# Performance work log

Hardware: AMD Instinct MI355X
Metric: run time of the kernel (lower is better)

## Reference

```python
import jax, jax.numpy as jnp
import numpy as np

# Clebsch-Gordan coefficients in the real basis; l=1 components stored in (y,z,x) order
S2 = 1.0 / np.sqrt(2.0)
S3 = 1.0 / np.sqrt(3.0)
S6 = 1.0 / np.sqrt(6.0)
_C2 = np.zeros((5, 3, 3), np.float32)
_C2[0, 2, 0] = _C2[0, 0, 2] = S2          # ~ xy
_C2[1, 0, 1] = _C2[1, 1, 0] = S2          # ~ yz
_C2[2, 1, 1] = 2.0 * S6                   # ~ 2z^2 - x^2 - y^2
_C2[2, 2, 2] = -S6
_C2[2, 0, 0] = -S6
_C2[3, 2, 1] = _C2[3, 1, 2] = S2          # ~ xz
_C2[4, 2, 2] = S2                          # ~ x^2 - y^2
_C2[4, 0, 0] = -S2
C2 = jnp.asarray(_C2)

N0, N1 = 64, 32        # multiplicities of input 0e / 1o irreps
CUTOFF = 5.0


def basis_functions(pos):
    """pos [N,3] -> (scalars [N,64], l=1 features [N,32,3])."""
    r = jnp.linalg.norm(pos, axis=-1, keepdims=True) + 1e-9        # [N,1]
    d = pos[:, (1, 2, 0)] / r                                       # unit dir, (y,z,x) order
    c0 = jnp.linspace(0.0, CUTOFF, N0, dtype=pos.dtype)
    c1 = jnp.linspace(0.0, CUTOFF, N1, dtype=pos.dtype)
    f0 = jnp.exp(-4.0 * (r - c0) ** 2)                              # [N,64] gaussian RBF
    f1 = jnp.exp(-4.0 * (r - c1) ** 2)                              # [N,32]
    x1 = f1[:, :, None] * d[:, None, :]                             # [N,32,3]
    return f0, x1


def lin_l(x, W):
    # channel mixing within one irrep block; preserves the m axis if present
    if x.ndim == 2:
        return x @ W
    return jnp.einsum('ncm,cd->ndm', x, W)


def tensor_product(a0, a1, b0, b1):
    """Full uvw CG tensor product of (64x0 + 32x1) x (64x0 + 32x1)."""
    N = a0.shape[0]
    # l=0 outputs: 0x0->0 and 1x1->0
    p000 = jnp.einsum('na,nb->nab', a0, b0).reshape(N, -1)                 # [N,4096]
    p110 = jnp.einsum('nam,nbm->nab', a1, b1).reshape(N, -1) * S3          # [N,1024]
    t0 = jnp.concatenate([p000, p110], axis=1)                             # [N,5120]
    # l=1 outputs: 0x1->1, 1x0->1, 1x1->1 (cross product)
    p011 = (a0[:, :, None, None] * b1[:, None, :, :]).reshape(N, -1, 3)    # [N,2048,3]
    p101 = (a1[:, :, None, :] * b0[:, None, :, None]).reshape(N, -1, 3)    # [N,2048,3]
    p111 = (jnp.cross(a1[:, :, None, :], b1[:, None, :, :]) * S2).reshape(N, -1, 3)
    t1 = jnp.concatenate([p011, p101, p111], axis=1)                       # [N,5120,3]
    # l=2 output: 1x1->2 via CG tensor
    t2 = jnp.einsum('nai,nbj,mij->nabm', a1, b1, C2).reshape(N, -1, 5)     # [N,1024,5]
    return t0, t1, t2


def setup_inputs() -> dict:
    key = jax.random.key(0)
    ks = jax.random.split(key, 10)
    N = 4096
    def w(k, i, o):
        return jax.random.normal(k, (i, o), jnp.float32) / np.sqrt(i)
    return {
        'positions': jax.random.normal(ks[0], (N, 3), jnp.float32) * 2.0,
        'W1_0': w(ks[1], 64, 64),
        'W1_1': w(ks[2], 32, 32),
        'W2_0': w(ks[3], 64, 64),
        'W2_1': w(ks[4], 32, 32),
        'W3_0': w(ks[5], 5120, 64),
        'W3_1': w(ks[6], 5120, 32),
        'W3_2': w(ks[7], 1024, 16),
        'W_out': w(ks[8], 240, 7),
        'b_out': jnp.zeros((7,), jnp.float32),
    }


def reference(positions, W1_0, W1_1, W2_0, W2_1, W3_0, W3_1, W3_2, W_out, b_out):
    f0, f1 = basis_functions(positions)                 # 64x0, 32x1
    a0, a1 = lin_l(f0, W1_0), lin_l(f1, W1_1)           # linear1
    b0, b1 = lin_l(f0, W2_0), lin_l(f1, W2_1)           # linear2
    t0, t1, t2 = tensor_product(a0, a1, b0, b1)         # 5120x0, 5120x1, 1024x2
    y0 = lin_l(t0, W3_0)                                # [N,64]
    y1 = lin_l(t1, W3_1)                                # [N,32,3]
    y2 = lin_l(t2, W3_2)                                # [N,16,5]
    N = y0.shape[0]
    feat = jnp.concatenate([y0, y1.reshape(N, -1), y2.reshape(N, -1)], axis=1)  # [N,240]
    return feat @ W_out + b_out                         # [N,7]
```

## Files before the change

### kernel.cpp

```cpp
#include <hip/hip_runtime.h>
#include <math.h>

#define NS2 0.70710678118654752440f
#define NS3 0.57735026918962576451f
#define NS6 0.40824829046386301636f

typedef _Float16 f16;
typedef _Float16 f16x8 __attribute__((ext_vector_type(8)));
typedef float    f32x4 __attribute__((ext_vector_type(4)));

#define GT_K    22528
#define UV_ROW  216
#define OFF_UV  360448
#define OFF_IDX 1245184

__global__ __launch_bounds__(256) void prep_kernel(
    const float* __restrict__ pos,
    const float* __restrict__ W1_0, const float* __restrict__ W1_1,
    const float* __restrict__ W2_0, const float* __restrict__ W2_1,
    const float* __restrict__ W3_0, const float* __restrict__ W3_1,
    const float* __restrict__ W3_2, const float* __restrict__ Wout,
    const float* __restrict__ bout,
    f16* __restrict__ wsh, float* __restrict__ out, int N)
{
    __shared__ float smem[2464];
    const int tid = threadIdx.x;

    if (blockIdx.x < 88) {
        float* s_wo = smem;
        for (int i = tid; i < 1680; i += 256) s_wo[i] = Wout[i];
        __syncthreads();
        int k = blockIdx.x * 256 + tid;
        float acc[7] = {0.f,0.f,0.f,0.f,0.f,0.f,0.f};
        if (k < 4096) {
            int a = k >> 6, b = k & 63;
            const float* wr = W3_0 + (a*64 + b) * 64;
            #pragma unroll 4
            for (int o = 0; o < 64; o += 4) {
                float4 wv = *(const float4*)(wr + o);
                const float* w0 = s_wo + o * 7;
                #pragma unroll
                for (int kk = 0; kk < 7; ++kk)
                    acc[kk] = fmaf(wv.x, w0[kk], fmaf(wv.y, w0[7+kk],
                              fmaf(wv.z, w0[14+kk], fmaf(wv.w, w0[21+kk], acc[kk]))));
            }
        } else if (k < 10240) {
            int it = k >> 6, s = it - 64, m = s >> 5, a2 = s & 31, l = k & 63;
            const float* wr = W3_1 + (2048 + a2*64 + l) * 32;
            #pragma unroll 4
            for (int o = 0; o < 32; o += 4) {
                float4 wv = *(const float4*)(wr + o);
                const float* w0 = s_wo + (64 + o*3 + m) * 7;
                #pragma unroll
                for (int kk = 0; kk < 7; ++kk)
                    acc[kk] = fmaf(wv.x, w0[kk], fmaf(wv.y, w0[21+kk],
                              fmaf(wv.z, w0[42+kk], fmaf(wv.w, w0[63+kk], acc[kk]))));
            }
        } else {
            int it2 = (k - 10240) >> 5, l32 = k & 31;
            if (it2 < 32) {
                const float* wr = W3_0 + (4096 + it2*32 + l32) * 64;
                #pragma unroll 4
                for (int o = 0; o < 64; o += 4) {
                    float4 wv = *(const float4*)(wr + o);
                    const float* w0 = s_wo + o * 7;
                    #pragma unroll
                    for (int kk = 0; kk < 7; ++kk)
                        acc[kk] = fmaf(wv.x, w0[kk], fmaf(wv.y, w0[7+kk],
                                  fmaf(wv.z, w0[14+kk], fmaf(wv.w, w0[21+kk], acc[kk]))));
                }
            } else if (it2 < 224) {
                int t = it2 - 32, m = t >> 6, a = t & 63;
                const float* wr = W3_1 + (a*32 + l32) * 32;
                #pragma unroll 4
                for (int o = 0; o < 32; o += 4) {
                    float4 wv = *(const float4*)(wr + o);
                    const float* w0 = s_wo + (64 + o*3 + m) * 7;
                    #pragma unroll
                    for (int kk = 0; kk < 7; ++kk)
                        acc[kk] = fmaf(wv.x, w0[kk], fmaf(wv.y, w0[21+kk],
                                  fmaf(wv.z, w0[42+kk], fmaf(wv.w, w0[63+kk], acc[kk]))));
                }
            } else {
                int t = it2 - 224, m = t >> 5, a = t & 31;
                const float* wr = W3_2 + (a*32 + l32) * 16;
                #pragma unroll 4
                for (int o = 0; o < 16; o += 4) {
                    float4 wv = *(const float4*)(wr + o);
                    const float* w0 = s_wo + (160 + o*5 + m) * 7;
                    #pragma unroll
                    for (int kk = 0; kk < 7; ++kk)
                        acc[kk] = fmaf(wv.x, w0[kk], fmaf(wv.y, w0[35+kk],
                                  fmaf(wv.z, w0[70+kk], fmaf(wv.w, w0[105+kk], acc[kk]))));
                }
            }
        }
        #pragma unroll
        for (int r = 0; r < 7; ++r)  wsh[(size_t)r * GT_K + k] = (f16)acc[r];
        #pragma unroll
        for (int r = 7; r < 16; ++r) wsh[(size_t)r * GT_K + k] = (f16)0.f;
        return;
    }

    if (blockIdx.x == 88 + 512) {
        for (int c = tid; c < 704; c += 256) {
            int uidx, gidx;
            if (c < 320) {
                int it = c >> 1;
                if (it < 64) { uidx = it; gidx = 9; }
                else { int s = it - 64; uidx = 64 + (s & 31); gidx = s >> 5; }
            } else {
                int it2 = c - 320;
                if (it2 < 32)       { uidx = 64 + it2;                gidx = 3; }
                else if (it2 < 224) { int t = it2 - 32;  uidx = t & 63;       gidx = t >> 6; }
                else                { int t = it2 - 224; uidx = 64 + (t & 31); gidx = 4 + (t >> 5); }
            }
            ((unsigned short*)(wsh + OFF_IDX))[c] = (unsigned short)(uidx | (gidx << 8));
        }
        return;
    }

    float* s_f0 = smem;
    float* s_f1 = smem + 512;
    const int g8   = blockIdx.x - 88;
    const int base = g8 * 8;
    f16* uv = wsh + OFF_UV;
    {
        int d = tid & 63;
        #pragma unroll
        for (int jj = 0; jj < 2; ++jj) {
            int j = (tid >> 6) + jj * 4;
            int n = base + j;
            float px = pos[n*3+0], py = pos[n*3+1], pz = pos[n*3+2];
            float r  = sqrtf(px*px + py*py + pz*pz) + 1e-9f;
            float t0 = r - (5.0f/63.0f) * (float)d;
            s_f0[j*64 + d] = __expf(-4.f * t0 * t0);
        }
        {
            int j = tid >> 5, d1 = tid & 31;
            int n = base + j;
            float px = pos[n*3+0], py = pos[n*3+1], pz = pos[n*3+2];
            float r  = sqrtf(px*px + py*py + pz*pz) + 1e-9f;
            float t1 = r - (5.0f/31.0f) * (float)d1;
            s_f1[j*32 + d1] = __expf(-4.f * t1 * t1);
        }
        if (tid < 8) {
            int n = base + tid;
            float px = pos[n*3+0], py = pos[n*3+1], pz = pos[n*3+2];
            float r  = sqrtf(px*px + py*py + pz*pz) + 1e-9f;
            float iv = 1.0f / r;
            float d0 = py*iv, d1 = pz*iv, d2 = px*iv;
            f16* row = uv + (size_t)n * UV_ROW;
            row[192+0] = (f16)d0;
            row[192+1] = (f16)d1;
            row[192+2] = (f16)d2;
            row[192+3] = (f16)(NS3 * (d0*d0 + d1*d1 + d2*d2));
            row[192+4] = (f16)(2.f*NS2*d2*d0);
            row[192+5] = (f16)(2.f*NS2*d0*d1);
            row[192+6] = (f16)(NS6*(2.f*d1*d1 - d2*d2 - d0*d0));
            row[192+7] = (f16)(2.f*NS2*d2*d1);
            row[192+8] = (f16)(NS2*(d2*d2 - d0*d0));
            row[201]   = (f16)1.0f;
        }
        if (tid < 56) out[base*7 + tid] = bout[tid % 7];
    }
    __syncthreads();
    {
        int c = tid & 63, jb = tid >> 6;
        float aa0 = 0.f, aa1 = 0.f, ba0 = 0.f, ba1 = 0.f;
        const float* wa = W1_0 + c;
        const float* wb = W2_0 + c;
        #pragma unroll 4
        for (int d = 0; d < 64; ++d) {
            float wav = wa[d*64], wbv = wb[d*64];
            float fA = s_f0[jb*64 + d], fB = s_f0[(jb+4)*64 + d];
            aa0 = fmaf(fA, wav, aa0);  aa1 = fmaf(fB, wav, aa1);
            ba0 = fmaf(fA, wbv, ba0);  ba1 = fmaf(fB, wbv, ba1);
        }
        uv[(size_t)(base+jb  )*UV_ROW +      c] = (f16)aa0;
        uv[(size_t)(base+jb+4)*UV_ROW +      c] = (f16)aa1;
        uv[(size_t)(base+jb  )*UV_ROW + 96 + c] = (f16)ba0;
        uv[(size_t)(base+jb+4)*UV_ROW + 96 + c] = (f16)ba1;

        int c1 = tid & 31, j8 = tid >> 5;
        float aA = 0.f, aB = 0.f;
        const float* wA = W1_1 + c1;
        const float* wB = W2_1 + c1;
        #pragma unroll 4
        for (int d = 0; d < 32; ++d) {
            float f = s_f1[j8*32 + d];
            aA = fmaf(f, wA[d*32], aA);
            aB = fmaf(f, wB[d*32], aB);
        }
        uv[(size_t)(base+j8)*UV_ROW +  64 + c1] = (f16)aA;
        uv[(size_t)(base+j8)*UV_ROW + 160 + c1] = (f16)aB;
    }
}

__global__ __launch_bounds__(256) void main_kernel(
    const f16* __restrict__ wsh, float* __restrict__ out, int N)
{
    __shared__ f16 s_g[2][16][264];
    __shared__ f16 s_uv[64][UV_ROW];
    __shared__ f16 s_ugt[2][64][8];
    __shared__ unsigned short s_idx[704];

    const int tid  = threadIdx.x;
    const int w    = tid >> 6;
    const int lane = tid & 63;
    const int lq   = lane >> 4;
    const int lm   = lane & 15;
    const int g    = blockIdx.x >> 3;
    const int kq   = blockIdx.x & 7;

    {
        const uint4* src = (const uint4*)(wsh + OFF_UV + (size_t)g * 64 * UV_ROW);
        uint4* dst = (uint4*)&s_uv[0][0];
        for (int j = tid; j < 1728; j += 256) dst[j] = src[j];
        const unsigned int* isrc = (const unsigned int*)(wsh + OFF_IDX);
        unsigned int* idst = (unsigned int*)s_idx;
        for (int j = tid; j < 352; j += 256) idst[j] = isrc[j];
    }
    __syncthreads();

    const f16* myrow = &s_uv[w*16 + lm][0];
    f16x8 vA0 = *(const f16x8*)(myrow +  96 + lq*8);
    f16x8 vA1 = *(const f16x8*)(myrow + 128 + lq*8);
    f16x8 vB  = *(const f16x8*)(myrow + 160 + lq*8);

    auto c0_of = [&](int t) {
        return (t < 5) ? (kq*40 + t*8) : (320 + kq*48 + (t-5)*8);
    };
    auto stage = [&](int t, int buf) {
        int c0 = c0_of(t), k0 = c0 * 32;
        const f16* src = wsh + k0;
        for (int j = tid; j < 512; j += 256) {
            int row = j >> 5, col = j & 31;
            uint4 v = *(const uint4*)(src + (size_t)row * GT_K + col*8);
            *(uint4*)&s_g[buf][row][col*8] = v;
        }
        for (int j = tid; j < 512; j += 256) {
            int n = j >> 3, s = j & 7;
            unsigned short ix = s_idx[c0 + s];
            float u  = (float)s_uv[n][ix & 255];
            float gg = (float)s_uv[n][192 + (ix >> 8)];
            s_ugt[buf][n][s] = (f16)(u * gg);
        }
    };

    f32x4 acc = {0.f, 0.f, 0.f, 0.f};
    auto compute = [&](int buf, bool isA) {
        #pragma unroll
        for (int s = 0; s < 8; ++s) {
            f16x8 a = *(const f16x8*)&s_g[buf][lm][s*32 + lq*8];
            f16 ug  = s_ugt[buf][w*16 + lm][s];
            f16x8 vv = isA ? ((s & 1) ? vA1 : vA0) : vB;
            f16x8 b;
            #pragma unroll
            for (int j2 = 0; j2 < 8; ++j2) b[j2] = vv[j2] * ug;
            acc = __builtin_amdgcn_mfma_f32_16x16x32_f16(a, b, acc, 0, 0, 0);
        }
    };

    stage(0, 0);
    __syncthreads();
    for (int t = 0; t < 11; ++t) {
        int buf = t & 1;
        if (t < 10) stage(t + 1, buf ^ 1);
        compute(buf, t < 5);
        __syncthreads();
    }

    int node = g*64 + w*16 + lm;
    if (lq == 0) {
        #pragma unroll
        for (int r = 0; r < 4; ++r) atomicAdd(&out[node*7 + r], acc[r]);
    } else if (lq == 1) {
        #pragma unroll
        for (int r = 0; r < 3; ++r) atomicAdd(&out[node*7 + 4 + r], acc[r]);
    }
}

extern "C" void kernel_launch(void* const* d_in, const int* in_sizes, int n_in,
                              void* d_out, int out_size, void* d_ws, size_t ws_size,
                              hipStream_t stream)
{
    const float* pos  = (const float*)d_in[0];
    const float* W1_0 = (const float*)d_in[1];
    const float* W1_1 = (const float*)d_in[2];
    const float* W2_0 = (const float*)d_in[3];
    const float* W2_1 = (const float*)d_in[4];
    const float* W3_0 = (const float*)d_in[5];
    const float* W3_1 = (const float*)d_in[6];
    const float* W3_2 = (const float*)d_in[7];
    const float* Wout = (const float*)d_in[8];
    const float* bout = (const float*)d_in[9];
    f16*   wsh = (f16*)d_ws;
    float* op  = (float*)d_out;
    int N = in_sizes[0] / 3;

    prep_kernel<<<88 + 512 + 1, 256, 0, stream>>>(pos, W1_0, W1_1, W2_0, W2_1,
                                                  W3_0, W3_1, W3_2, Wout, bout, wsh, op, N);
    main_kernel<<<512, 256, 0, stream>>>(wsh, op, N);
}
```

Measured before the change: 100.7 us.

## Split folded-weight precompute across 4x more blocks and shrink padded weight tile

The folded W3·Wout precompute now uses 64 outputs per block, with four threads splitting each reduction and combining partials through shared memory. This spreads work over 352 blocks instead of 88, shortening the serial per-thread reductions in the prep kernel. The workspace no longer stores 9 zero-padding rows: main_kernel stages only 7 real rows plus one zeroed shared row, and clamps the MFMA A-row index to it. The index table is also computed inside each main_kernel block rather than read from a separate workspace region.

New measurement: 96.14 us. 1.05x faster.

```diff
diff --git a/kernel.cpp b/kernel.cpp
--- a/kernel.cpp
+++ b/kernel.cpp
@@ -11,8 +11,7 @@
 
 #define GT_K    22528
 #define UV_ROW  216
-#define OFF_UV  360448
-#define OFF_IDX 1245184
+#define OFF_UV  157696
 
 __global__ __launch_bounds__(256) void prep_kernel(
     const float* __restrict__ pos,
@@ -23,20 +22,22 @@
     const float* __restrict__ bout,
     f16* __restrict__ wsh, float* __restrict__ out, int N)
 {
-    __shared__ float smem[2464];
+    __shared__ float smem[3728];
     const int tid = threadIdx.x;
 
-    if (blockIdx.x < 88) {
-        float* s_wo = smem;
+    if (blockIdx.x < 352) {
+        float* s_wo  = smem;
+        float* s_red = smem + 1680;
         for (int i = tid; i < 1680; i += 256) s_wo[i] = Wout[i];
         __syncthreads();
-        int k = blockIdx.x * 256 + tid;
+        const int kl = tid & 63, q = tid >> 6;
+        const int k  = blockIdx.x * 64 + kl;
         float acc[7] = {0.f,0.f,0.f,0.f,0.f,0.f,0.f};
         if (k < 4096) {
-            int a = k >> 6, b = k & 63;
-            const float* wr = W3_0 + (a*64 + b) * 64;
-            #pragma unroll 4
-            for (int o = 0; o < 64; o += 4) {
+            const float* wr = W3_0 + (size_t)k * 64;
+            #pragma unroll
+            for (int oo = 0; oo < 16; oo += 4) {
+                int o = q*16 + oo;
                 float4 wv = *(const float4*)(wr + o);
                 const float* w0 = s_wo + o * 7;
                 #pragma unroll
@@ -46,9 +47,10 @@
             }
         } else if (k < 10240) {
             int it = k >> 6, s = it - 64, m = s >> 5, a2 = s & 31, l = k & 63;
-            const float* wr = W3_1 + (2048 + a2*64 + l) * 32;
-            #pragma unroll 4
-            for (int o = 0; o < 32; o += 4) {
+            const float* wr = W3_1 + (size_t)(2048 + a2*64 + l) * 32;
+            #pragma unroll
+            for (int oo = 0; oo < 8; oo += 4) {
+                int o = q*8 + oo;
                 float4 wv = *(const float4*)(wr + o);
                 const float* w0 = s_wo + (64 + o*3 + m) * 7;
                 #pragma unroll
@@ -59,9 +61,10 @@
         } else {
             int it2 = (k - 10240) >> 5, l32 = k & 31;
             if (it2 < 32) {
-                const float* wr = W3_0 + (4096 + it2*32 + l32) * 64;
-                #pragma unroll 4
-                for (int o = 0; o < 64; o += 4) {
+                const float* wr = W3_0 + (size_t)(4096 + it2*32 + l32) * 64;
+                #pragma unroll
+                for (int oo = 0; oo < 16; oo += 4) {
+                    int o = q*16 + oo;
                     float4 wv = *(const float4*)(wr + o);
                     const float* w0 = s_wo + o * 7;
                     #pragma unroll
@@ -71,9 +74,10 @@
                 }
             } else if (it2 < 224) {
                 int t = it2 - 32, m = t >> 6, a = t & 63;
-                const float* wr = W3_1 + (a*32 + l32) * 32;
-                #pragma unroll 4
-                for (int o = 0; o < 32; o += 4) {
+                const float* wr = W3_1 + (size_t)(a*32 + l32) * 32;
+                #pragma unroll
+                for (int oo = 0; oo < 8; oo += 4) {
+                    int o = q*8 + oo;
                     float4 wv = *(const float4*)(wr + o);
                     const float* w0 = s_wo + (64 + o*3 + m) * 7;
                     #pragma unroll
@@ -83,46 +87,33 @@
                 }
             } else {
                 int t = it2 - 224, m = t >> 5, a = t & 31;
-                const float* wr = W3_2 + (a*32 + l32) * 16;
-                #pragma unroll 4
-                for (int o = 0; o < 16; o += 4) {
-                    float4 wv = *(const float4*)(wr + o);
-                    const float* w0 = s_wo + (160 + o*5 + m) * 7;
-                    #pragma unroll
-                    for (int kk = 0; kk < 7; ++kk)
-                        acc[kk] = fmaf(wv.x, w0[kk], fmaf(wv.y, w0[35+kk],
-                                  fmaf(wv.z, w0[70+kk], fmaf(wv.w, w0[105+kk], acc[kk]))));
-                }
-            }
-        }
-        #pragma unroll
-        for (int r = 0; r < 7; ++r)  wsh[(size_t)r * GT_K + k] = (f16)acc[r];
-        #pragma unroll
-        for (int r = 7; r < 16; ++r) wsh[(size_t)r * GT_K + k] = (f16)0.f;
-        return;
-    }
-
-    if (blockIdx.x == 88 + 512) {
-        for (int c = tid; c < 704; c += 256) {
-            int uidx, gidx;
-            if (c < 320) {
-                int it = c >> 1;
-                if (it < 64) { uidx = it; gidx = 9; }
-                else { int s = it - 64; uidx = 64 + (s & 31); gidx = s >> 5; }
-            } else {
-                int it2 = c - 320;
-                if (it2 < 32)       { uidx = 64 + it2;                gidx = 3; }
-                else if (it2 < 224) { int t = it2 - 32;  uidx = t & 63;       gidx = t >> 6; }
-                else                { int t = it2 - 224; uidx = 64 + (t & 31); gidx = 4 + (t >> 5); }
-            }
-            ((unsigned short*)(wsh + OFF_IDX))[c] = (unsigned short)(uidx | (gidx << 8));
+                const float* wr = W3_2 + (size_t)(a*32 + l32) * 16;
+                int o = q*4;
+                float4 wv = *(const float4*)(wr + o);
+                const float* w0 = s_wo + (160 + o*5 + m) * 7;
+                #pragma unroll
+                for (int kk = 0; kk < 7; ++kk)
+                    acc[kk] = fmaf(wv.x, w0[kk], fmaf(wv.y, w0[35+kk],
+                              fmaf(wv.z, w0[70+kk], fmaf(wv.w, w0[105+kk], acc[kk]))));
+            }
+        }
+        #pragma unroll
+        for (int r = 0; r < 7; ++r) s_red[(q*64 + kl)*8 + r] = acc[r];
+        __syncthreads();
+        if (tid < 64) {
+            #pragma unroll
+            for (int r = 0; r < 7; ++r) {
+                float v = s_red[(      tid)*8 + r] + s_red[( 64 + tid)*8 + r]
+                        + s_red[(128 + tid)*8 + r] + s_red[(192 + tid)*8 + r];
+                wsh[(size_t)r * GT_K + blockIdx.x*64 + tid] = (f16)v;
+            }
         }
         return;
     }
 
     float* s_f0 = smem;
     float* s_f1 = smem + 512;
-    const int g8   = blockIdx.x - 88;
+    const int g8   = blockIdx.x - 352;
     const int base = g8 * 8;
     f16* uv = wsh + OFF_UV;
     {
@@ -200,7 +191,7 @@
 __global__ __launch_bounds__(256) void main_kernel(
     const f16* __restrict__ wsh, float* __restrict__ out, int N)
 {
-    __shared__ f16 s_g[2][16][264];
+    __shared__ f16 s_g[2][8][264];
     __shared__ f16 s_uv[64][UV_ROW];
     __shared__ f16 s_ugt[2][64][8];
     __shared__ unsigned short s_idx[704];
@@ -210,6 +201,7 @@
     const int lane = tid & 63;
     const int lq   = lane >> 4;
     const int lm   = lane & 15;
+    const int ra   = (lm < 7) ? lm : 7;
     const int g    = blockIdx.x >> 3;
     const int kq   = blockIdx.x & 7;
 
@@ -217,9 +209,24 @@
         const uint4* src = (const uint4*)(wsh + OFF_UV + (size_t)g * 64 * UV_ROW);
         uint4* dst = (uint4*)&s_uv[0][0];
         for (int j = tid; j < 1728; j += 256) dst[j] = src[j];
-        const unsigned int* isrc = (const unsigned int*)(wsh + OFF_IDX);
-        unsigned int* idst = (unsigned int*)s_idx;
-        for (int j = tid; j < 352; j += 256) idst[j] = isrc[j];
+        for (int c = tid; c < 704; c += 256) {
+            int uidx, gidx;
+            if (c < 320) {
+                int it = c >> 1;
+                if (it < 64) { uidx = it; gidx = 9; }
+                else { int s = it - 64; uidx = 64 + (s & 31); gidx = s >> 5; }
+            } else {
+                int it2 = c - 320;
+                if (it2 < 32)       { uidx = 64 + it2;                 gidx = 3; }
+                else if (it2 < 224) { int t = it2 - 32;  uidx = t & 63;        gidx = t >> 6; }
+                else                { int t = it2 - 224; uidx = 64 + (t & 31); gidx = 4 + (t >> 5); }
+            }
+            s_idx[c] = (unsigned short)(uidx | (gidx << 8));
+        }
+        for (int i = tid; i < 264; i += 256) {
+            s_g[0][7][i] = (f16)0.f;
+            s_g[1][7][i] = (f16)0.f;
+        }
     }
     __syncthreads();
 
@@ -234,7 +241,7 @@
     auto stage = [&](int t, int buf) {
         int c0 = c0_of(t), k0 = c0 * 32;
         const f16* src = wsh + k0;
-        for (int j = tid; j < 512; j += 256) {
+        for (int j = tid; j < 224; j += 256) {
             int row = j >> 5, col = j & 31;
             uint4 v = *(const uint4*)(src + (size_t)row * GT_K + col*8);
             *(uint4*)&s_g[buf][row][col*8] = v;
@@ -252,7 +259,7 @@
     auto compute = [&](int buf, bool isA) {
         #pragma unroll
         for (int s = 0; s < 8; ++s) {
-            f16x8 a = *(const f16x8*)&s_g[buf][lm][s*32 + lq*8];
+            f16x8 a = *(const f16x8*)&s_g[buf][ra][s*32 + lq*8];
             f16 ug  = s_ugt[buf][w*16 + lm][s];
             f16x8 vv = isA ? ((s & 1) ? vA1 : vA0) : vB;
             f16x8 b;
@@ -299,7 +306,7 @@
     float* op  = (float*)d_out;
     int N = in_sizes[0] / 3;
 
-    prep_kernel<<<88 + 512 + 1, 256, 0, stream>>>(pos, W1_0, W1_1, W2_0, W2_1,
-                                                  W3_0, W3_1, W3_2, Wout, bout, wsh, op, N);
+    prep_kernel<<<352 + N/8, 256, 0, stream>>>(pos, W1_0, W1_1, W2_0, W2_1,
+                                               W3_0, W3_1, W3_2, Wout, bout, wsh, op, N);
     main_kernel<<<512, 256, 0, stream>>>(wsh, op, N);
 }
```
